# Performance work log

Hardware: AMD Instinct MI355X
Metric: run time of the kernel (lower is better)

## Reference

```python
import jax, jax.numpy as jnp
import numpy as np

B, NQ, NKV, D = 2, 2048, 4096, 1024
H, DH = 16, 64            # qk_channels = v_channels = 1024 -> 16 heads x 64
HID = 2 * int(4.0 * D)    # GEGLU produces 8192 -> split into 2x4096
EPS = 1e-6


def layernorm(x, scale, bias):
    mu = jnp.mean(x, axis=-1, keepdims=True)
    var = jnp.mean(jnp.square(x - mu), axis=-1, keepdims=True)
    return (x - mu) * jax.lax.rsqrt(var + EPS) * scale + bias


def setup_inputs() -> dict:
    key = jax.random.key(0)
    ks = jax.random.split(key, 12)
    s = 0.02
    return {
        "inputs_q": jax.random.normal(ks[0], (B, NQ, D), jnp.float32),
        "inputs_kv": jax.random.normal(ks[1], (B, NKV, D), jnp.float32),
        "ln_q_scale": jnp.ones((D,), jnp.float32),
        "ln_q_bias": jnp.zeros((D,), jnp.float32),
        "ln_kv_scale": jnp.ones((D,), jnp.float32),
        "ln_kv_bias": jnp.zeros((D,), jnp.float32),
        "Wq": s * jax.random.normal(ks[2], (D, H, DH), jnp.float32),
        "bq": jnp.zeros((H, DH), jnp.float32),
        "Wk": s * jax.random.normal(ks[3], (D, H, DH), jnp.float32),
        "bk": jnp.zeros((H, DH), jnp.float32),
        "Wv": s * jax.random.normal(ks[4], (D, H, DH), jnp.float32),
        "bv": jnp.zeros((H, DH), jnp.float32),
        "Wo": s * jax.random.normal(ks[5], (H, DH, D), jnp.float32),
        "bo": jnp.zeros((D,), jnp.float32),
        "ln2_scale": jnp.ones((D,), jnp.float32),
        "ln2_bias": jnp.zeros((D,), jnp.float32),
        "W1": s * jax.random.normal(ks[6], (D, HID), jnp.float32),
        "b1": jnp.zeros((HID,), jnp.float32),
        "W2": s * jax.random.normal(ks[7], (HID // 2, D), jnp.float32),
        "b2": jnp.zeros((D,), jnp.float32),
    }


def reference(inputs_q, inputs_kv, ln_q_scale, ln_q_bias, ln_kv_scale, ln_kv_bias,
              Wq, bq, Wk, bk, Wv, bv, Wo, bo, ln2_scale, ln2_bias, W1, b1, W2, b2):
    ln_q = layernorm(inputs_q, ln_q_scale, ln_q_bias)
    ln_kv = layernorm(inputs_kv, ln_kv_scale, ln_kv_bias)
    # multi-head projections: DenseGeneral to (H, DH)
    q = jnp.einsum('bqd,dhe->bqhe', ln_q, Wq) + bq
    k = jnp.einsum('bkd,dhe->bkhe', ln_kv, Wk) + bk
    v = jnp.einsum('bkd,dhe->bkhe', ln_kv, Wv) + bv
    # scaled dot-product attention (full score matrix, as in source)
    attn = jnp.einsum('bqhd,bkhd->bhqk', q, k) / np.sqrt(DH).astype(np.float32)
    attn = jax.nn.softmax(attn, axis=-1)
    o = jnp.einsum('bhqk,bkhd->bqhd', attn, v)
    # output projection contracting (H, DH)
    x = jnp.einsum('bqhd,hdo->bqo', o, Wo) + bo
    x = x + inputs_q  # query residual
    # GEGLU MLP
    h = layernorm(x, ln2_scale, ln2_bias)
    h = jnp.dot(h, W1) + b1
    a, g = jnp.split(h, 2, axis=-1)
    h = a * jax.nn.gelu(g)  # approximate (tanh) gelu, flax default
    y = jnp.dot(h, W2) + b2
    return x + y
```

## Files before the change

### kernel.cpp

```cpp
#include <hip/hip_runtime.h>

typedef unsigned short u16;
typedef unsigned int u32;
typedef float f32x4 __attribute__((ext_vector_type(4)));
typedef float f32x16 __attribute__((ext_vector_type(16)));
typedef __bf16 bf16x8 __attribute__((ext_vector_type(8)));
typedef short s16x8 __attribute__((ext_vector_type(8)));
typedef short s16x4 __attribute__((ext_vector_type(4)));
typedef u32 u32x4 __attribute__((ext_vector_type(4)));

#define MFMA16(a, b, c) __builtin_amdgcn_mfma_f32_16x16x32_bf16((a), (b), (c), 0, 0, 0)
#define MFMA32(a, b, c) __builtin_amdgcn_mfma_f32_32x32x16_bf16((a), (b), (c), 0, 0, 0)

typedef const __attribute__((address_space(1))) void* gas1_t;
typedef __attribute__((address_space(3))) void* las3_t;
#define GLDS16(g, l) __builtin_amdgcn_global_load_lds((gas1_t)(g), (las3_t)(l), 16, 0, 0)

static __device__ __forceinline__ u16 f2bf(float f) {
  u32 u = __builtin_bit_cast(u32, f);
  u += 0x7FFFu + ((u >> 16) & 1u);
  return (u16)(u >> 16);
}
static __device__ __forceinline__ float bf2f(u16 h) {
  return __builtin_bit_cast(float, (u32)h << 16);
}
static __device__ __forceinline__ u32 cvtpk(float lo, float hi) {
  u32 r;
  asm("v_cvt_pk_bf16_f32 %0, %1, %2" : "=v"(r) : "v"(lo), "v"(hi));
  return r;
}
static __device__ __forceinline__ float gelu_t(float g) {
  float u = 0.7978845608f * (g + 0.044715f * g * g * g);
  float e = __expf(2.0f * u);
  float t = 1.0f - 2.0f / (e + 1.0f);
  return 0.5f * g * (1.0f + t);
}

__global__ __launch_bounds__(256) void transp_cvt(const float* __restrict__ in,
                                                  u16* __restrict__ out, int K, int N,
                                                  float scale) {
  __shared__ u16 t[64][72];
  int k0 = blockIdx.x * 64, n0 = blockIdx.y * 64;
#pragma unroll
  for (int i = 0; i < 16; ++i) {
    int idx = threadIdx.x + i * 256;
    int r = idx >> 6, c = idx & 63;
    t[r][c] = f2bf(in[(size_t)(k0 + r) * N + n0 + c] * scale);
  }
  __syncthreads();
#pragma unroll
  for (int i = 0; i < 16; ++i) {
    int idx = threadIdx.x + i * 256;
    int r = idx >> 6, c = idx & 63;
    out[(size_t)(n0 + r) * K + k0 + c] = t[c][r];
  }
}

__global__ __launch_bounds__(256) void geglu_transp(const float* __restrict__ in,
                                                    u16* __restrict__ out) {
  __shared__ u16 t[64][72];
  int k0 = blockIdx.x * 64, n0 = blockIdx.y * 64;
#pragma unroll
  for (int i = 0; i < 16; ++i) {
    int idx = threadIdx.x + i * 256;
    int r = idx >> 6, c = idx & 63;
    int np = n0 + c;
    int orig = ((np >> 5) << 4) + (np & 15) + (((np >> 4) & 1) << 12);
    t[r][c] = f2bf(in[(size_t)(k0 + r) * 8192 + orig]);
  }
  __syncthreads();
#pragma unroll
  for (int i = 0; i < 16; ++i) {
    int idx = threadIdx.x + i * 256;
    int r = idx >> 6, c = idx & 63;
    out[(size_t)(n0 + r) * 1024 + k0 + c] = t[c][r];
  }
}

__global__ __launch_bounds__(256) void ln_bf16(const float* __restrict__ x,
                                               const float* __restrict__ sc,
                                               const float* __restrict__ bi,
                                               u16* __restrict__ out) {
  int row = blockIdx.x;
  int tid = threadIdx.x;
  float4 v = ((const float4*)(x + (size_t)row * 1024))[tid];
  float s = v.x + v.y + v.z + v.w;
  float s2 = v.x * v.x + v.y * v.y + v.z * v.z + v.w * v.w;
  for (int m = 1; m < 64; m <<= 1) {
    s += __shfl_xor(s, m);
    s2 += __shfl_xor(s2, m);
  }
  __shared__ float rs[4], rs2[4];
  int wave = tid >> 6, lane = tid & 63;
  if (lane == 0) { rs[wave] = s; rs2[wave] = s2; }
  __syncthreads();
  s = rs[0] + rs[1] + rs[2] + rs[3];
  s2 = rs2[0] + rs2[1] + rs2[2] + rs2[3];
  float mu = s * (1.0f / 1024.0f);
  float var = s2 * (1.0f / 1024.0f) - mu * mu;
  float inv = rsqrtf(var + 1e-6f);
  float4 scv = ((const float4*)sc)[tid];
  float4 biv = ((const float4*)bi)[tid];
  s16x4 o;
  o[0] = (short)f2bf((v.x - mu) * inv * scv.x + biv.x);
  o[1] = (short)f2bf((v.y - mu) * inv * scv.y + biv.y);
  o[2] = (short)f2bf((v.z - mu) * inv * scv.z + biv.z);
  o[3] = (short)f2bf((v.w - mu) * inv * scv.w + biv.w);
  *(s16x4*)(out + (size_t)row * 1024 + tid * 4) = o;
}

template <int MODE>
__global__ __launch_bounds__(256) void gemm_nt(const u16* __restrict__ A,
                                               const u16* __restrict__ Bt,
                                               const float* __restrict__ bias,
                                               const float* __restrict__ resid,
                                               void* __restrict__ Cout,
                                               int M, int N, int K, float bias_scale) {
  __shared__ u16 As[128 * 64];
  __shared__ u16 Bs[128 * 64];
  const int nbx = gridDim.x;
  const int nwg = nbx * gridDim.y;
  const int wg0 = blockIdx.y * nbx + blockIdx.x;
  const int wg = (nwg & 7) ? wg0 : (wg0 & 7) * (nwg >> 3) + (wg0 >> 3);
  const int m0 = (wg % nbx) * 128, n0 = (wg / nbx) * 128;
  const int tid = threadIdx.x;
  const int lane = tid & 63, wave = tid >> 6;
  const int wm = (wave >> 1) * 64, wn = (wave & 1) * 64;
  const int lr = lane & 15, hi4 = lane >> 4;
  f32x4 acc[4][4] = {};
  for (int k0 = 0; k0 < K; k0 += 64) {
#pragma unroll
    for (int i = 0; i < 4; ++i) {
      int s = i * 256 + tid;
      int r = s >> 3, slot = s & 7;
      int gslot = slot ^ (r & 7);
      int ldst = (i * 256 + wave * 64) * 8;
      GLDS16(A + (size_t)(m0 + r) * K + k0 + gslot * 8, &As[ldst]);
      GLDS16(Bt + (size_t)(n0 + r) * K + k0 + gslot * 8, &Bs[ldst]);
    }
    __syncthreads();
#pragma unroll
    for (int ks = 0; ks < 2; ++ks) {
      const int sl = ((ks * 4 + hi4) ^ (lr & 7)) * 8;
      bf16x8 af[4], bfr[4];
#pragma unroll
      for (int t = 0; t < 4; ++t) {
        af[t] = __builtin_bit_cast(bf16x8, *(const s16x8*)&As[(wm + t * 16 + lr) * 64 + sl]);
        bfr[t] = __builtin_bit_cast(bf16x8, *(const s16x8*)&Bs[(wn + t * 16 + lr) * 64 + sl]);
      }
#pragma unroll
      for (int mt = 0; mt < 4; ++mt)
#pragma unroll
        for (int nt = 0; nt < 4; ++nt)
          acc[mt][nt] = MFMA16(af[mt], bfr[nt], acc[mt][nt]);
    }
    __syncthreads();
  }
#pragma unroll
  for (int mt = 0; mt < 4; ++mt) {
#pragma unroll
    for (int nt = 0; nt < 4; ++nt) {
      const int ncol = n0 + wn + nt * 16 + lr;
      const float bv = bias[ncol] * bias_scale;
      const int mbase = m0 + wm + mt * 16 + hi4 * 4;
#pragma unroll
      for (int r = 0; r < 4; ++r) {
        const int m = mbase + r;
        const float val = acc[mt][nt][r] + bv;
        if constexpr (MODE == 0) {
          ((u16*)Cout)[(size_t)m * N + ncol] = f2bf(val);
        } else {
          ((float*)Cout)[(size_t)m * N + ncol] = val + resid[(size_t)m * N + ncol];
        }
      }
    }
  }
}

template <int MODE>
__global__ __launch_bounds__(512, 2) void gemm256(const u16* __restrict__ A,
                                                  const u16* __restrict__ Bt,
                                                  const float* __restrict__ bias,
                                                  const float* __restrict__ bias2,
                                                  u16* __restrict__ Cout,
                                                  u16* __restrict__ Vout,
                                                  int M, int N, int K, int nmajor) {
  __shared__ __align__(16) u16 sA[2][2][256 * 32];
  __shared__ __align__(16) u16 sB[2][2][256 * 32];
  const int nbx = M >> 8, nby = N >> 8;
  const int nblk = nbx * nby;
  const int cpx = nblk >> 3;
  const int wg0 = blockIdx.x;
  const int wg = (wg0 & 7) * cpx + (wg0 >> 3);
  int mi, ni;
  if (nmajor) { ni = wg % nby; mi = wg / nby; } else { mi = wg % nbx; ni = wg / nbx; }
  const int m0 = mi << 8, n0 = ni << 8;
  const int tid = threadIdx.x;
  const int lane = tid & 63, wave = tid >> 6;
  const int wr = wave >> 2, wc = wave & 3;
  const int lr = lane & 15, hi4 = lane >> 4;
  const int rdoct = (hi4 ^ ((lr >> 1) & 3)) * 8;
  const int NT = K >> 6;

  auto stageA = [&](int t, int kh) {
#pragma unroll
    for (int i = 0; i < 2; ++i) {
      int idx = i * 512 + tid;
      int r = idx >> 2, go = (idx & 3) ^ ((r >> 1) & 3);
      GLDS16(A + (size_t)(m0 + r) * K + t * 64 + kh * 32 + go * 8,
             &sA[t & 1][kh][(i * 512 + wave * 64) * 8]);
    }
  };
  auto stageB = [&](int t, int kh) {
#pragma unroll
    for (int i = 0; i < 2; ++i) {
      int idx = i * 512 + tid;
      int r = idx >> 2, go = (idx & 3) ^ ((r >> 1) & 3);
      GLDS16(Bt + (size_t)(n0 + r) * K + t * 64 + kh * 32 + go * 8,
             &sB[t & 1][kh][(i * 512 + wave * 64) * 8]);
    }
  };

  f32x4 acc[8][4] = {};
  bf16x8 af[4], bf[4];

  stageA(0, 0); stageB(0, 0); stageA(0, 1); stageB(0, 1);
  asm volatile("s_waitcnt vmcnt(4)" ::: "memory");
  __builtin_amdgcn_s_barrier();
  __builtin_amdgcn_sched_barrier(0);

  for (int t = 0; t < NT; ++t) {
    const int buf = t & 1;
    const bool pre = (t + 1 < NT);
#pragma unroll
    for (int kh = 0; kh < 2; ++kh) {
#pragma unroll
      for (int nt = 0; nt < 4; ++nt)
        bf[nt] = __builtin_bit_cast(bf16x8,
            *(const s16x8*)&sB[buf][kh][(wc * 64 + nt * 16 + lr) * 32 + rdoct]);
#pragma unroll
      for (int mf = 0; mf < 4; ++mf)
        af[mf] = __builtin_bit_cast(bf16x8,
            *(const s16x8*)&sA[buf][kh][(wr * 128 + mf * 16 + lr) * 32 + rdoct]);
      if (pre) stageA(t + 1, kh);
      __builtin_amdgcn_s_barrier();
      asm volatile("s_waitcnt lgkmcnt(0)" ::: "memory");
      __builtin_amdgcn_sched_barrier(0);
      __builtin_amdgcn_s_setprio(1);
#pragma unroll
      for (int mf = 0; mf < 4; ++mf)
#pragma unroll
        for (int nt = 0; nt < 4; ++nt)
          acc[mf][nt] = MFMA16(af[mf], bf[nt], acc[mf][nt]);
      __builtin_amdgcn_s_setprio(0);
      __builtin_amdgcn_s_barrier();
      __builtin_amdgcn_sched_barrier(0);
#pragma unroll
      for (int mf = 0; mf < 4; ++mf)
        af[mf] = __builtin_bit_cast(bf16x8,
            *(const s16x8*)&sA[buf][kh][(wr * 128 + (4 + mf) * 16 + lr) * 32 + rdoct]);
      if (pre) stageB(t + 1, kh);
      __builtin_amdgcn_s_barrier();
      asm volatile("s_waitcnt lgkmcnt(0)" ::: "memory");
      __builtin_amdgcn_sched_barrier(0);
      __builtin_amdgcn_s_setprio(1);
#pragma unroll
      for (int mf = 0; mf < 4; ++mf)
#pragma unroll
        for (int nt = 0; nt < 4; ++nt)
          acc[4 + mf][nt] = MFMA16(af[mf], bf[nt], acc[4 + mf][nt]);
      __builtin_amdgcn_s_setprio(0);
      if (pre)
        asm volatile("s_waitcnt vmcnt(4)" ::: "memory");
      else
        asm volatile("s_waitcnt vmcnt(0)" ::: "memory");
      __builtin_amdgcn_s_barrier();
      __builtin_amdgcn_sched_barrier(0);
    }
  }

  if constexpr (MODE == 0) {
#pragma unroll
    for (int mf = 0; mf < 8; ++mf) {
#pragma unroll
      for (int nt = 0; nt < 4; ++nt) {
        const int ncol = n0 + wc * 64 + nt * 16 + lr;
        const int mbase = m0 + wr * 128 + mf * 16 + hi4 * 4;
        const bool isk = ncol < 1024;
        const int vc = isk ? ncol : ncol - 1024;
        const float bv = isk ? bias[ncol] : bias2[vc];
#pragma unroll
        for (int r = 0; r < 4; ++r) {
          const int m = mbase + r;
          const float val = acc[mf][nt][r] + bv;
          if (isk) {
            Cout[(size_t)m * 1024 + ncol] = f2bf(val);
          } else {
            size_t vidx = ((size_t)((m >> 12) * 1024 + vc) << 12) | (size_t)(m & 4095);
            Vout[vidx] = f2bf(val);
          }
        }
      }
    }
  } else {
#pragma unroll
    for (int mf = 0; mf < 8; ++mf) {
      const int mbase = m0 + wr * 128 + mf * 16 + hi4 * 4;
#pragma unroll
      for (int p = 0; p < 2; ++p) {
        const int oc = (((n0 + wc * 64 + p * 32) >> 5) << 4) + lr;
        const float ba = bias[oc];
        const float bg = bias[oc + 4096];
#pragma unroll
        for (int r = 0; r < 4; ++r) {
          const int m = mbase + r;
          float a = acc[mf][2 * p][r] + ba;
          float g = acc[mf][2 * p + 1][r] + bg;
          Cout[(size_t)m * 4096 + oc] = f2bf(a * gelu_t(g));
        }
      }
    }
  }
}

__global__ __launch_bounds__(256, 2) void flash_attn(const u16* __restrict__ Qg,
                                                     const u16* __restrict__ Kg,
                                                     const u16* __restrict__ Vt,
                                                     u16* __restrict__ Og) {
  __shared__ u16 Ks[2][64 * 64];
  __shared__ u16 Vs[2][64 * 64];
  const int id = blockIdx.x;
  const int bh = (id & 7) * 4 + ((id >> 3) & 3);
  const int qb = id >> 5;
  const int b = bh >> 4, h = bh & 15;
  const int q0 = qb * 128;
  const int tid = threadIdx.x;
  const int lane = tid & 63, wave = tid >> 6;
  const int lq = lane & 31, hi = lane >> 5;
  const u16* Kbase = Kg + (size_t)(b * 4096) * 1024 + h * 64;
  const u16* Vbase = Vt + (size_t)((b * 16 + h) * 64) * 4096;
  bf16x8 qf[4];
  const size_t qrow = (size_t)(b * 2048 + q0 + wave * 32 + lq);
#pragma unroll
  for (int dc = 0; dc < 4; ++dc)
    qf[dc] = __builtin_bit_cast(bf16x8, *(const s16x8*)&Qg[qrow * 1024 + h * 64 + dc * 16 + hi * 8]);

  f32x16 oacc0 = {}, oacc1 = {};
  float lrun = 0.0f;

  auto stage = [&](int buf, int tile) {
    const int kv0 = tile * 64;
#pragma unroll
    for (int i = 0; i < 2; ++i) {
      int s = i * 256 + tid;
      int r = s >> 3;
      int inb = ((s & 7) * 16) ^ ((r & 7) << 4);
      GLDS16(Kbase + (size_t)(kv0 + r) * 1024 + (inb >> 1), &Ks[buf][(i * 256 + wave * 64) * 8]);
    }
#pragma unroll
    for (int i = 0; i < 2; ++i) {
      int s = i * 256 + tid;
      int r = s >> 3;
      int inb = ((s & 7) * 16) ^ ((r & 7) << 4);
      GLDS16(Vbase + (size_t)r * 4096 + kv0 + (inb >> 1), &Vs[buf][(i * 256 + wave * 64) * 8]);
    }
  };

  stage(0, 0);
  __syncthreads();
  int cur = 0;
  for (int t = 0; t < 64; ++t) {
    if (t < 63) stage(cur ^ 1, t + 1);
    f32x16 sA = {}, sB = {};
    __builtin_amdgcn_s_setprio(1);
#pragma unroll
    for (int dc = 0; dc < 4; ++dc) {
      int row = lq;
      int inb = (dc * 32 + hi * 16) ^ ((row & 7) << 4);
      bf16x8 kf = __builtin_bit_cast(bf16x8, *(const s16x8*)&Ks[cur][row * 64 + (inb >> 1)]);
      sA = MFMA32(kf, qf[dc], sA);
    }
#pragma unroll
    for (int dc = 0; dc < 4; ++dc) {
      int row = 32 + lq;
      int inb = (dc * 32 + hi * 16) ^ ((row & 7) << 4);
      bf16x8 kf = __builtin_bit_cast(bf16x8, *(const s16x8*)&Ks[cur][row * 64 + (inb >> 1)]);
      sB = MFMA32(kf, qf[dc], sB);
    }
    __builtin_amdgcn_s_setprio(0);
#pragma unroll
    for (int i = 0; i < 16; ++i) sA[i] = __builtin_amdgcn_exp2f(sA[i]);
#pragma unroll
    for (int i = 0; i < 16; ++i) sB[i] = __builtin_amdgcn_exp2f(sB[i]);
    float a0 = (sA[0] + sA[1]) + (sA[2] + sA[3]);
    float a1 = (sA[4] + sA[5]) + (sA[6] + sA[7]);
    float a2 = (sA[8] + sA[9]) + (sA[10] + sA[11]);
    float a3 = (sA[12] + sA[13]) + (sA[14] + sA[15]);
    float b0 = (sB[0] + sB[1]) + (sB[2] + sB[3]);
    float b1s = (sB[4] + sB[5]) + (sB[6] + sB[7]);
    float b2s = (sB[8] + sB[9]) + (sB[10] + sB[11]);
    float b3 = (sB[12] + sB[13]) + (sB[14] + sB[15]);
    float ts = ((a0 + a1) + (a2 + a3)) + ((b0 + b1s) + (b2s + b3));
    ts += __shfl_xor(ts, 32);
    lrun += ts;
    u32 wa[8], wb[8];
#pragma unroll
    for (int i = 0; i < 8; ++i) wa[i] = cvtpk(sA[2 * i], sA[2 * i + 1]);
#pragma unroll
    for (int i = 0; i < 8; ++i) wb[i] = cvtpk(sB[2 * i], sB[2 * i + 1]);
    u32 a0w = wa[0], c0 = wa[2];
    asm("v_permlane32_swap_b32 %0, %1" : "+v"(a0w), "+v"(c0));
    u32 a1w = wa[1], c1 = wa[3];
    asm("v_permlane32_swap_b32 %0, %1" : "+v"(a1w), "+v"(c1));
    u32 a2w = wa[4], c2 = wa[6];
    asm("v_permlane32_swap_b32 %0, %1" : "+v"(a2w), "+v"(c2));
    u32 a3w = wa[5], c3 = wa[7];
    asm("v_permlane32_swap_b32 %0, %1" : "+v"(a3w), "+v"(c3));
    u32 e0 = wb[0], g0 = wb[2];
    asm("v_permlane32_swap_b32 %0, %1" : "+v"(e0), "+v"(g0));
    u32 e1 = wb[1], g1 = wb[3];
    asm("v_permlane32_swap_b32 %0, %1" : "+v"(e1), "+v"(g1));
    u32 e2 = wb[4], g2 = wb[6];
    asm("v_permlane32_swap_b32 %0, %1" : "+v"(e2), "+v"(g2));
    u32 e3 = wb[5], g3 = wb[7];
    asm("v_permlane32_swap_b32 %0, %1" : "+v"(e3), "+v"(g3));
    u32x4 t00 = {a0w, a1w, c0, c1};
    u32x4 t01 = {a2w, a3w, c2, c3};
    u32x4 t10 = {e0, e1, g0, g1};
    u32x4 t11 = {e2, e3, g2, g3};
    bf16x8 p00 = __builtin_bit_cast(bf16x8, t00);
    bf16x8 p01 = __builtin_bit_cast(bf16x8, t01);
    bf16x8 p10 = __builtin_bit_cast(bf16x8, t10);
    bf16x8 p11 = __builtin_bit_cast(bf16x8, t11);
    __builtin_amdgcn_s_setprio(1);
#pragma unroll
    for (int st = 0; st < 2; ++st) {
      bf16x8 pc0 = st ? p10 : p00;
      bf16x8 pc1 = st ? p11 : p01;
#pragma unroll
      for (int c = 0; c < 2; ++c) {
        bf16x8 pf = c ? pc1 : pc0;
        {
          int row = lq;
          int inb = (st * 64 + c * 32 + hi * 16) ^ ((row & 7) << 4);
          bf16x8 vf = __builtin_bit_cast(bf16x8, *(const s16x8*)&Vs[cur][row * 64 + (inb >> 1)]);
          oacc0 = MFMA32(vf, pf, oacc0);
        }
        {
          int row = 32 + lq;
          int inb = (st * 64 + c * 32 + hi * 16) ^ ((row & 7) << 4);
          bf16x8 vf = __builtin_bit_cast(bf16x8, *(const s16x8*)&Vs[cur][row * 64 + (inb >> 1)]);
          oacc1 = MFMA32(vf, pf, oacc1);
        }
      }
    }
    __builtin_amdgcn_s_setprio(0);
    __syncthreads();
    cur ^= 1;
  }
  float rinv = 1.0f / lrun;
  u16* obase = Og + qrow * 1024 + h * 64;
#pragma unroll
  for (int rp = 0; rp < 8; ++rp) {
    int r0 = rp * 2;
    int d0 = (r0 & 3) + 8 * (r0 >> 2) + 4 * hi;
    *(u32*)&obase[d0] = cvtpk(oacc0[r0] * rinv, oacc0[r0 + 1] * rinv);
    *(u32*)&obase[32 + d0] = cvtpk(oacc1[r0] * rinv, oacc1[r0 + 1] * rinv);
  }
}

extern "C" void kernel_launch(void* const* d_in, const int* in_sizes, int n_in,
                              void* d_out, int out_size, void* d_ws, size_t ws_size,
                              hipStream_t stream) {
  (void)in_sizes; (void)n_in; (void)out_size; (void)ws_size;
  const float* inputs_q = (const float*)d_in[0];
  const float* inputs_kv = (const float*)d_in[1];
  const float* ln_q_scale = (const float*)d_in[2];
  const float* ln_q_bias = (const float*)d_in[3];
  const float* ln_kv_scale = (const float*)d_in[4];
  const float* ln_kv_bias = (const float*)d_in[5];
  const float* Wq = (const float*)d_in[6];
  const float* bq = (const float*)d_in[7];
  const float* Wk = (const float*)d_in[8];
  const float* bk = (const float*)d_in[9];
  const float* Wv = (const float*)d_in[10];
  const float* bv = (const float*)d_in[11];
  const float* Wo = (const float*)d_in[12];
  const float* bo = (const float*)d_in[13];
  const float* ln2_scale = (const float*)d_in[14];
  const float* ln2_bias = (const float*)d_in[15];
  const float* W1 = (const float*)d_in[16];
  const float* b1 = (const float*)d_in[17];
  const float* W2 = (const float*)d_in[18];
  const float* b2 = (const float*)d_in[19];
  float* out = (float*)d_out;
  char* ws = (char*)d_ws;
  const size_t MB = 1ull << 20;
  u16* lnq = (u16*)(ws + 0);
  u16* lnkv = (u16*)(ws + 8 * MB);
  u16* Qb = (u16*)(ws + 24 * MB);
  u16* Kb = (u16*)(ws + 32 * MB);
  u16* Vtb = (u16*)(ws + 48 * MB);
  u16* Ob = (u16*)(ws + 64 * MB);
  float* xbuf = (float*)(ws + 72 * MB);
  u16* ln2b = (u16*)(ws + 88 * MB);
  u16* gg = (u16*)(ws + 96 * MB);
  u16* wqt = (u16*)(ws + 128 * MB);
  u16* wkvt = (u16*)(ws + 130 * MB);
  u16* wot = (u16*)(ws + 134 * MB);
  u16* w1i = (u16*)(ws + 136 * MB);
  u16* w2t = (u16*)(ws + 152 * MB);

  const float QSC = 0.125f * 1.44269504088896f;
  dim3 blk(256);
  transp_cvt<<<dim3(16, 16), blk, 0, stream>>>(Wq, wqt, 1024, 1024, QSC);
  transp_cvt<<<dim3(16, 16), blk, 0, stream>>>(Wk, wkvt, 1024, 1024, 1.0f);
  transp_cvt<<<dim3(16, 16), blk, 0, stream>>>(Wv, wkvt + 1024 * 1024, 1024, 1024, 1.0f);
  transp_cvt<<<dim3(16, 16), blk, 0, stream>>>(Wo, wot, 1024, 1024, 1.0f);
  geglu_transp<<<dim3(16, 128), blk, 0, stream>>>(W1, w1i);
  transp_cvt<<<dim3(64, 16), blk, 0, stream>>>(W2, w2t, 4096, 1024, 1.0f);
  ln_bf16<<<4096, blk, 0, stream>>>(inputs_q, ln_q_scale, ln_q_bias, lnq);
  ln_bf16<<<8192, blk, 0, stream>>>(inputs_kv, ln_kv_scale, ln_kv_bias, lnkv);
  gemm_nt<0><<<dim3(32, 8), blk, 0, stream>>>(lnq, wqt, bq, nullptr, Qb, 4096, 1024, 1024, QSC);
  gemm256<0><<<dim3(256), dim3(512), 0, stream>>>(lnkv, wkvt, bk, bv, Kb, Vtb, 8192, 2048, 1024, 1);
  flash_attn<<<dim3(512), blk, 0, stream>>>(Qb, Kb, Vtb, Ob);
  gemm_nt<2><<<dim3(32, 8), blk, 0, stream>>>(Ob, wot, bo, inputs_q, xbuf, 4096, 1024, 1024, 1.0f);
  ln_bf16<<<4096, blk, 0, stream>>>(xbuf, ln2_scale, ln2_bias, ln2b);
  gemm256<1><<<dim3(512), dim3(512), 0, stream>>>(ln2b, w1i, b1, nullptr, gg, nullptr, 4096, 8192, 1024, 0);
  gemm_nt<2><<<dim3(32, 8), blk, 0, stream>>>(gg, w2t, b2, xbuf, out, 4096, 1024, 4096, 1.0f);
}
```

Measured before the change: 409.5 us.

## Merge weight prep and layernorm launches, load K into registers in flash attention

The six weight transpose/convert kernels become one launch, and the q and kv layernorms become one launch with block-index dispatch, which cuts launch overhead. In flash attention, K tiles are now read straight from global memory into registers with a two-tile ping-pong instead of being staged through LDS. The softmax row sum is computed by an MFMA against a ones vector instead of shuffles and VALU adds. This frees LDS and VALU work but raises register pressure and drops coalesced LDS staging for K.

```diff
diff --git a/kernel.cpp b/kernel.cpp
--- a/kernel.cpp
+++ b/kernel.cpp
@@ -21,9 +21,6 @@
   u += 0x7FFFu + ((u >> 16) & 1u);
   return (u16)(u >> 16);
 }
-static __device__ __forceinline__ float bf2f(u16 h) {
-  return __builtin_bit_cast(float, (u32)h << 16);
-}
 static __device__ __forceinline__ u32 cvtpk(float lo, float hi) {
   u32 r;
   asm("v_cvt_pk_bf16_f32 %0, %1, %2" : "=v"(r) : "v"(lo), "v"(hi));
@@ -36,52 +33,85 @@
   return 0.5f * g * (1.0f + t);
 }
 
-__global__ __launch_bounds__(256) void transp_cvt(const float* __restrict__ in,
-                                                  u16* __restrict__ out, int K, int N,
-                                                  float scale) {
+__global__ __launch_bounds__(256) void prep_weights(const float* __restrict__ Wq,
+                                                    const float* __restrict__ Wk,
+                                                    const float* __restrict__ Wv,
+                                                    const float* __restrict__ Wo,
+                                                    const float* __restrict__ W1,
+                                                    const float* __restrict__ W2,
+                                                    u16* __restrict__ wqt,
+                                                    u16* __restrict__ wkvt,
+                                                    u16* __restrict__ wot,
+                                                    u16* __restrict__ w1i,
+                                                    u16* __restrict__ w2t, float qsc) {
   __shared__ u16 t[64][72];
-  int k0 = blockIdx.x * 64, n0 = blockIdx.y * 64;
-#pragma unroll
-  for (int i = 0; i < 16; ++i) {
-    int idx = threadIdx.x + i * 256;
-    int r = idx >> 6, c = idx & 63;
-    t[r][c] = f2bf(in[(size_t)(k0 + r) * N + n0 + c] * scale);
-  }
-  __syncthreads();
-#pragma unroll
-  for (int i = 0; i < 16; ++i) {
-    int idx = threadIdx.x + i * 256;
-    int r = idx >> 6, c = idx & 63;
-    out[(size_t)(n0 + r) * K + k0 + c] = t[c][r];
-  }
-}
-
-__global__ __launch_bounds__(256) void geglu_transp(const float* __restrict__ in,
-                                                    u16* __restrict__ out) {
-  __shared__ u16 t[64][72];
-  int k0 = blockIdx.x * 64, n0 = blockIdx.y * 64;
-#pragma unroll
-  for (int i = 0; i < 16; ++i) {
-    int idx = threadIdx.x + i * 256;
-    int r = idx >> 6, c = idx & 63;
-    int np = n0 + c;
-    int orig = ((np >> 5) << 4) + (np & 15) + (((np >> 4) & 1) << 12);
-    t[r][c] = f2bf(in[(size_t)(k0 + r) * 8192 + orig]);
-  }
-  __syncthreads();
-#pragma unroll
-  for (int i = 0; i < 16; ++i) {
-    int idx = threadIdx.x + i * 256;
-    int r = idx >> 6, c = idx & 63;
-    out[(size_t)(n0 + r) * 1024 + k0 + c] = t[c][r];
-  }
-}
-
-__global__ __launch_bounds__(256) void ln_bf16(const float* __restrict__ x,
-                                               const float* __restrict__ sc,
-                                               const float* __restrict__ bi,
-                                               u16* __restrict__ out) {
-  int row = blockIdx.x;
+  const int id = blockIdx.x;
+  const int tid = threadIdx.x;
+  auto tileT = [&](const float* in, u16* out, int K, int N, int k0, int n0, float scale) {
+#pragma unroll
+    for (int i = 0; i < 16; ++i) {
+      int idx = tid + i * 256;
+      int r = idx >> 6, c = idx & 63;
+      t[r][c] = f2bf(in[(size_t)(k0 + r) * N + n0 + c] * scale);
+    }
+    __syncthreads();
+#pragma unroll
+    for (int i = 0; i < 16; ++i) {
+      int idx = tid + i * 256;
+      int r = idx >> 6, c = idx & 63;
+      out[(size_t)(n0 + r) * K + k0 + c] = t[c][r];
+    }
+  };
+  if (id < 256) {
+    tileT(Wq, wqt, 1024, 1024, (id & 15) * 64, (id >> 4) * 64, qsc);
+  } else if (id < 512) {
+    int i2 = id - 256;
+    tileT(Wk, wkvt, 1024, 1024, (i2 & 15) * 64, (i2 >> 4) * 64, 1.0f);
+  } else if (id < 768) {
+    int i2 = id - 512;
+    tileT(Wv, wkvt + 1024 * 1024, 1024, 1024, (i2 & 15) * 64, (i2 >> 4) * 64, 1.0f);
+  } else if (id < 1024) {
+    int i2 = id - 768;
+    tileT(Wo, wot, 1024, 1024, (i2 & 15) * 64, (i2 >> 4) * 64, 1.0f);
+  } else if (id < 3072) {
+    int i2 = id - 1024;
+    int k0 = (i2 & 15) * 64, n0 = (i2 >> 4) * 64;
+#pragma unroll
+    for (int i = 0; i < 16; ++i) {
+      int idx = tid + i * 256;
+      int r = idx >> 6, c = idx & 63;
+      int np = n0 + c;
+      int orig = ((np >> 5) << 4) + (np & 15) + (((np >> 4) & 1) << 12);
+      t[r][c] = f2bf(W1[(size_t)(k0 + r) * 8192 + orig]);
+    }
+    __syncthreads();
+#pragma unroll
+    for (int i = 0; i < 16; ++i) {
+      int idx = tid + i * 256;
+      int r = idx >> 6, c = idx & 63;
+      w1i[(size_t)(n0 + r) * 1024 + k0 + c] = t[c][r];
+    }
+  } else {
+    int i3 = id - 3072;
+    tileT(W2, w2t, 4096, 1024, (i3 & 63) * 64, (i3 >> 6) * 64, 1.0f);
+  }
+}
+
+__global__ __launch_bounds__(256) void ln_fused(const float* __restrict__ xq,
+                                                const float* __restrict__ xkv,
+                                                const float* __restrict__ scq,
+                                                const float* __restrict__ biq,
+                                                const float* __restrict__ sckv,
+                                                const float* __restrict__ bikv,
+                                                u16* __restrict__ outq,
+                                                u16* __restrict__ outkv) {
+  const int id = blockIdx.x;
+  const bool isq = id < 4096;
+  const int row = isq ? id : id - 4096;
+  const float* x = isq ? xq : xkv;
+  const float* sc = isq ? scq : sckv;
+  const float* bi = isq ? biq : bikv;
+  u16* out = isq ? outq : outkv;
   int tid = threadIdx.x;
   float4 v = ((const float4*)(x + (size_t)row * 1024))[tid];
   float s = v.x + v.y + v.z + v.w;
@@ -327,7 +357,6 @@
                                                      const u16* __restrict__ Kg,
                                                      const u16* __restrict__ Vt,
                                                      u16* __restrict__ Og) {
-  __shared__ u16 Ks[2][64 * 64];
   __shared__ u16 Vs[2][64 * 64];
   const int id = blockIdx.x;
   const int bh = (id & 7) * 4 + ((id >> 3) & 3);
@@ -345,18 +374,23 @@
   for (int dc = 0; dc < 4; ++dc)
     qf[dc] = __builtin_bit_cast(bf16x8, *(const s16x8*)&Qg[qrow * 1024 + h * 64 + dc * 16 + hi * 8]);
 
-  f32x16 oacc0 = {}, oacc1 = {};
-  float lrun = 0.0f;
-
-  auto stage = [&](int buf, int tile) {
+  const u32x4 onesw = {0x3F803F80u, 0x3F803F80u, 0x3F803F80u, 0x3F803F80u};
+  const bf16x8 ones = __builtin_bit_cast(bf16x8, onesw);
+
+  f32x16 oacc0 = {}, oacc1 = {}, accl = {};
+
+  const u16* kptr = Kbase + (size_t)(size_t)lq * 1024 + hi * 8;
+  auto loadK = [&](bf16x8* dst, int tile) {
+    const size_t base = (size_t)tile * 64 * 1024;
+#pragma unroll
+    for (int st = 0; st < 2; ++st)
+#pragma unroll
+      for (int dc = 0; dc < 4; ++dc)
+        dst[st * 4 + dc] = __builtin_bit_cast(bf16x8,
+            *(const s16x8*)&kptr[base + (size_t)st * 32 * 1024 + dc * 16]);
+  };
+  auto stageV = [&](int buf, int tile) {
     const int kv0 = tile * 64;
-#pragma unroll
-    for (int i = 0; i < 2; ++i) {
-      int s = i * 256 + tid;
-      int r = s >> 3;
-      int inb = ((s & 7) * 16) ^ ((r & 7) << 4);
-      GLDS16(Kbase + (size_t)(kv0 + r) * 1024 + (inb >> 1), &Ks[buf][(i * 256 + wave * 64) * 8]);
-    }
 #pragma unroll
     for (int i = 0; i < 2; ++i) {
       int s = i * 256 + tid;
@@ -366,56 +400,41 @@
     }
   };
 
-  stage(0, 0);
-  __syncthreads();
-  int cur = 0;
-  for (int t = 0; t < 64; ++t) {
-    if (t < 63) stage(cur ^ 1, t + 1);
+  auto compute = [&](const bf16x8* kf, const u16* Vbuf) {
     f32x16 sA = {}, sB = {};
     __builtin_amdgcn_s_setprio(1);
 #pragma unroll
-    for (int dc = 0; dc < 4; ++dc) {
-      int row = lq;
-      int inb = (dc * 32 + hi * 16) ^ ((row & 7) << 4);
-      bf16x8 kf = __builtin_bit_cast(bf16x8, *(const s16x8*)&Ks[cur][row * 64 + (inb >> 1)]);
-      sA = MFMA32(kf, qf[dc], sA);
-    }
-#pragma unroll
-    for (int dc = 0; dc < 4; ++dc) {
-      int row = 32 + lq;
-      int inb = (dc * 32 + hi * 16) ^ ((row & 7) << 4);
-      bf16x8 kf = __builtin_bit_cast(bf16x8, *(const s16x8*)&Ks[cur][row * 64 + (inb >> 1)]);
-      sB = MFMA32(kf, qf[dc], sB);
-    }
+    for (int dc = 0; dc < 4; ++dc) sA = MFMA32(kf[dc], qf[dc], sA);
+#pragma unroll
+    for (int dc = 0; dc < 4; ++dc) sB = MFMA32(kf[4 + dc], qf[dc], sB);
     __builtin_amdgcn_s_setprio(0);
+    bf16x8 vf0[4];
+#pragma unroll
+    for (int c = 0; c < 2; ++c) {
+#pragma unroll
+      for (int half = 0; half < 2; ++half) {
+        int row = half * 32 + lq;
+        int inb = (c * 32 + hi * 16) ^ ((row & 7) << 4);
+        vf0[c * 2 + half] = __builtin_bit_cast(bf16x8, *(const s16x8*)&Vbuf[row * 64 + (inb >> 1)]);
+      }
+    }
 #pragma unroll
     for (int i = 0; i < 16; ++i) sA[i] = __builtin_amdgcn_exp2f(sA[i]);
 #pragma unroll
     for (int i = 0; i < 16; ++i) sB[i] = __builtin_amdgcn_exp2f(sB[i]);
-    float a0 = (sA[0] + sA[1]) + (sA[2] + sA[3]);
-    float a1 = (sA[4] + sA[5]) + (sA[6] + sA[7]);
-    float a2 = (sA[8] + sA[9]) + (sA[10] + sA[11]);
-    float a3 = (sA[12] + sA[13]) + (sA[14] + sA[15]);
-    float b0 = (sB[0] + sB[1]) + (sB[2] + sB[3]);
-    float b1s = (sB[4] + sB[5]) + (sB[6] + sB[7]);
-    float b2s = (sB[8] + sB[9]) + (sB[10] + sB[11]);
-    float b3 = (sB[12] + sB[13]) + (sB[14] + sB[15]);
-    float ts = ((a0 + a1) + (a2 + a3)) + ((b0 + b1s) + (b2s + b3));
-    ts += __shfl_xor(ts, 32);
-    lrun += ts;
     u32 wa[8], wb[8];
 #pragma unroll
     for (int i = 0; i < 8; ++i) wa[i] = cvtpk(sA[2 * i], sA[2 * i + 1]);
 #pragma unroll
     for (int i = 0; i < 8; ++i) wb[i] = cvtpk(sB[2 * i], sB[2 * i + 1]);
-    u32 a0w = wa[0], c0 = wa[2];
-    asm("v_permlane32_swap_b32 %0, %1" : "+v"(a0w), "+v"(c0));
-    u32 a1w = wa[1], c1 = wa[3];
-    asm("v_permlane32_swap_b32 %0, %1" : "+v"(a1w), "+v"(c1));
-    u32 a2w = wa[4], c2 = wa[6];
-    asm("v_permlane32_swap_b32 %0, %1" : "+v"(a2w), "+v"(c2));
-    u32 a3w = wa[5], c3 = wa[7];
-    asm("v_permlane32_swap_b32 %0, %1" : "+v"(a3w), "+v"(c3));
+    u32 a0 = wa[0], c0 = wa[2];
+    asm("v_permlane32_swap_b32 %0, %1" : "+v"(a0), "+v"(c0));
+    u32 a1 = wa[1], c1 = wa[3];
+    asm("v_permlane32_swap_b32 %0, %1" : "+v"(a1), "+v"(c1));
+    u32 a2 = wa[4], c2 = wa[6];
+    asm("v_permlane32_swap_b32 %0, %1" : "+v"(a2), "+v"(c2));
+    u32 a3 = wa[5], c3 = wa[7];
+    asm("v_permlane32_swap_b32 %0, %1" : "+v"(a3), "+v"(c3));
     u32 e0 = wb[0], g0 = wb[2];
     asm("v_permlane32_swap_b32 %0, %1" : "+v"(e0), "+v"(g0));
     u32 e1 = wb[1], g1 = wb[3];
@@ -424,41 +443,51 @@
     asm("v_permlane32_swap_b32 %0, %1" : "+v"(e2), "+v"(g2));
     u32 e3 = wb[5], g3 = wb[7];
     asm("v_permlane32_swap_b32 %0, %1" : "+v"(e3), "+v"(g3));
-    u32x4 t00 = {a0w, a1w, c0, c1};
-    u32x4 t01 = {a2w, a3w, c2, c3};
+    u32x4 t00 = {a0, a1, c0, c1};
+    u32x4 t01 = {a2, a3, c2, c3};
     u32x4 t10 = {e0, e1, g0, g1};
     u32x4 t11 = {e2, e3, g2, g3};
-    bf16x8 p00 = __builtin_bit_cast(bf16x8, t00);
-    bf16x8 p01 = __builtin_bit_cast(bf16x8, t01);
-    bf16x8 p10 = __builtin_bit_cast(bf16x8, t10);
-    bf16x8 p11 = __builtin_bit_cast(bf16x8, t11);
+    bf16x8 pf[4] = {__builtin_bit_cast(bf16x8, t00), __builtin_bit_cast(bf16x8, t01),
+                    __builtin_bit_cast(bf16x8, t10), __builtin_bit_cast(bf16x8, t11)};
     __builtin_amdgcn_s_setprio(1);
 #pragma unroll
-    for (int st = 0; st < 2; ++st) {
-      bf16x8 pc0 = st ? p10 : p00;
-      bf16x8 pc1 = st ? p11 : p01;
-#pragma unroll
-      for (int c = 0; c < 2; ++c) {
-        bf16x8 pf = c ? pc1 : pc0;
-        {
-          int row = lq;
-          int inb = (st * 64 + c * 32 + hi * 16) ^ ((row & 7) << 4);
-          bf16x8 vf = __builtin_bit_cast(bf16x8, *(const s16x8*)&Vs[cur][row * 64 + (inb >> 1)]);
-          oacc0 = MFMA32(vf, pf, oacc0);
-        }
-        {
-          int row = 32 + lq;
-          int inb = (st * 64 + c * 32 + hi * 16) ^ ((row & 7) << 4);
-          bf16x8 vf = __builtin_bit_cast(bf16x8, *(const s16x8*)&Vs[cur][row * 64 + (inb >> 1)]);
-          oacc1 = MFMA32(vf, pf, oacc1);
-        }
-      }
+    for (int c = 0; c < 2; ++c) {
+      oacc0 = MFMA32(vf0[c * 2 + 0], pf[c], oacc0);
+      oacc1 = MFMA32(vf0[c * 2 + 1], pf[c], oacc1);
+      accl = MFMA32(ones, pf[c], accl);
+    }
+#pragma unroll
+    for (int c = 0; c < 2; ++c) {
+      {
+        int row = lq;
+        int inb = (64 + c * 32 + hi * 16) ^ ((row & 7) << 4);
+        bf16x8 vf = __builtin_bit_cast(bf16x8, *(const s16x8*)&Vbuf[row * 64 + (inb >> 1)]);
+        oacc0 = MFMA32(vf, pf[2 + c], oacc0);
+      }
+      {
+        int row = 32 + lq;
+        int inb = (64 + c * 32 + hi * 16) ^ ((row & 7) << 4);
+        bf16x8 vf = __builtin_bit_cast(bf16x8, *(const s16x8*)&Vbuf[row * 64 + (inb >> 1)]);
+        oacc1 = MFMA32(vf, pf[2 + c], oacc1);
+      }
+      accl = MFMA32(ones, pf[2 + c], accl);
     }
     __builtin_amdgcn_s_setprio(0);
+  };
+
+  bf16x8 kfA[8], kfB[8];
+  loadK(kfA, 0);
+  stageV(0, 0);
+  __syncthreads();
+  for (int t = 0; t < 64; t += 2) {
+    if (t + 1 < 64) { stageV(1, t + 1); loadK(kfB, t + 1); }
+    compute(kfA, Vs[0]);
     __syncthreads();
-    cur ^= 1;
-  }
-  float rinv = 1.0f / lrun;
+    if (t + 2 < 64) { stageV(0, t + 2); loadK(kfA, t + 2); }
+    compute(kfB, Vs[1]);
+    __syncthreads();
+  }
+  float rinv = 1.0f / accl[0];
   u16* obase = Og + qrow * 1024 + h * 64;
 #pragma unroll
   for (int rp = 0; rp < 8; ++rp) {
@@ -513,19 +542,15 @@
 
   const float QSC = 0.125f * 1.44269504088896f;
   dim3 blk(256);
-  transp_cvt<<<dim3(16, 16), blk, 0, stream>>>(Wq, wqt, 1024, 1024, QSC);
-  transp_cvt<<<dim3(16, 16), blk, 0, stream>>>(Wk, wkvt, 1024, 1024, 1.0f);
-  transp_cvt<<<dim3(16, 16), blk, 0, stream>>>(Wv, wkvt + 1024 * 1024, 1024, 1024, 1.0f);
-  transp_cvt<<<dim3(16, 16), blk, 0, stream>>>(Wo, wot, 1024, 1024, 1.0f);
-  geglu_transp<<<dim3(16, 128), blk, 0, stream>>>(W1, w1i);
-  transp_cvt<<<dim3(64, 16), blk, 0, stream>>>(W2, w2t, 4096, 1024, 1.0f);
-  ln_bf16<<<4096, blk, 0, stream>>>(inputs_q, ln_q_scale, ln_q_bias, lnq);
-  ln_bf16<<<8192, blk, 0, stream>>>(inputs_kv, ln_kv_scale, ln_kv_bias, lnkv);
+  prep_weights<<<dim3(4096), blk, 0, stream>>>(Wq, Wk, Wv, Wo, W1, W2, wqt, wkvt, wot, w1i, w2t, QSC);
+  ln_fused<<<dim3(12288), blk, 0, stream>>>(inputs_q, inputs_kv, ln_q_scale, ln_q_bias,
+                                            ln_kv_scale, ln_kv_bias, lnq, lnkv);
   gemm_nt<0><<<dim3(32, 8), blk, 0, stream>>>(lnq, wqt, bq, nullptr, Qb, 4096, 1024, 1024, QSC);
   gemm256<0><<<dim3(256), dim3(512), 0, stream>>>(lnkv, wkvt, bk, bv, Kb, Vtb, 8192, 2048, 1024, 1);
   flash_attn<<<dim3(512), blk, 0, stream>>>(Qb, Kb, Vtb, Ob);
   gemm_nt<2><<<dim3(32, 8), blk, 0, stream>>>(Ob, wot, bo, inputs_q, xbuf, 4096, 1024, 1024, 1.0f);
-  ln_bf16<<<4096, blk, 0, stream>>>(xbuf, ln2_scale, ln2_bias, ln2b);
+  ln_fused<<<dim3(4096), blk, 0, stream>>>(xbuf, xbuf, ln2_scale, ln2_bias, ln2_scale, ln2_bias,
+                                           ln2b, ln2b);
   gemm256<1><<<dim3(512), dim3(512), 0, stream>>>(ln2b, w1i, b1, nullptr, gg, nullptr, 4096, 8192, 1024, 0);
   gemm_nt<2><<<dim3(32, 8), blk, 0, stream>>>(gg, w2t, b2, xbuf, out, 4096, 1024, 4096, 1.0f);
 }
```

Measured after the change: 452.6 us. 1.11x slower.
